# Performance work log

Hardware: AMD Instinct MI355X
Metric: run time of the kernel (lower is better)

The kernel has to match this reference:

```python
import jax, jax.numpy as jnp
import numpy as np

NEG_SLOPE = 0.01  # torch F.leaky_relu default


def _gcn_conv(x, edge_index, Wc, bc):
    """PyG GCNConv with add_self_loops + symmetric normalization.
    x: [N, F], edge_index: [2, E] (row=source, col=target)."""
    N = x.shape[0]
    xw = x @ Wc  # transform first, then propagate
    loop = jnp.arange(N, dtype=edge_index.dtype)
    src = jnp.concatenate([edge_index[0], loop])
    dst = jnp.concatenate([edge_index[1], loop])
    deg = jax.ops.segment_sum(jnp.ones(src.shape[0], xw.dtype), dst, num_segments=N)
    dinv = jnp.where(deg > 0, jax.lax.rsqrt(deg), 0.0)
    norm = dinv[src] * dinv[dst]  # [E+N]
    agg = jax.ops.segment_sum(norm[:, None] * xw[src], dst, num_segments=N)
    return agg + bc


def setup_inputs() -> dict:
    key = jax.random.key(0)
    ks = jax.random.split(key, 6)
    B, N, E, F, H = 8, 10000, 160000, 128, 256
    node_features = jax.random.normal(ks[0], (B, N, F), dtype=jnp.float32)
    edge_index = jax.random.randint(ks[1], (B, 2, E), 0, N, dtype=jnp.int64)
    Wc = jax.random.normal(ks[2], (F, F), dtype=jnp.float32) / np.sqrt(F)
    bc = jnp.zeros((F,), jnp.float32)
    W1 = jax.random.normal(ks[3], (F, H), dtype=jnp.float32) / np.sqrt(F)
    b1 = jnp.zeros((H,), jnp.float32)
    W2 = jax.random.normal(ks[4], (H, H), dtype=jnp.float32) / np.sqrt(H)
    b2 = jnp.zeros((H,), jnp.float32)
    return {"node_features": node_features, "edge_index": edge_index,
            "Wc": Wc, "bc": bc, "W1": W1, "b1": b1, "W2": W2, "b2": b2}


def reference(node_features, edge_index, Wc, bc, W1, b1, W2, b2):
    # vmapped per-graph GCN conv (equivalent to PyG Batch with node offsets)
    conv = jax.vmap(_gcn_conv, in_axes=(0, 0, None, None))
    x0 = node_features  # [B, N, F]
    x = jax.nn.relu(conv(x0, edge_index, Wc, bc))
    x = x + x0  # residual with raw input (batch.x)
    x = jax.nn.leaky_relu(x @ W1 + b1, NEG_SLOPE)
    x = jax.nn.leaky_relu(x @ W2 + b2, NEG_SLOPE)
    return x  # [B, N, H]
```

## Files before the change

### kernel.cpp

```cpp
#include <hip/hip_runtime.h>
#include <hip/hip_bf16.h>
#include <hip/hip_fp16.h>

#define Bn 8
#define Nn 10000
#define En 160000
#define Fn 128
#define Hn 256
#define NROW (Bn * Nn)
#define NEDGE (Bn * En)
#define TM 32

#define OFF_RS   80000
#define OFF_CUR  160004
#define OFF_BS   240004
#define OFF_BO   240320
#define OFF_EP   240832
#define WSI_END  2800832
#define WP_U16   131072
#define WP_BYTES ((size_t)WP_U16 * 2)
#define X0H_BYTES ((size_t)NROW * Fn * 2)
#define X0H_OFF  ((size_t)WSI_END * 4 + WP_BYTES)
#define WS_NEED  (X0H_OFF + X0H_BYTES)

typedef unsigned short u16;
typedef __attribute__((ext_vector_type(8))) short s16x8;
typedef __attribute__((ext_vector_type(8))) _Float16 f16x8;
typedef __attribute__((ext_vector_type(4))) float f32x4;

__device__ __forceinline__ u16 f2bf(float x) {
    unsigned u = __float_as_uint(x);
    u += 0x7FFF + ((u >> 16) & 1);
    return (u16)(u >> 16);
}
__device__ __forceinline__ float bf2f(u16 h) {
    return __uint_as_float((unsigned)h << 16);
}
__device__ __forceinline__ u16 f2h(float x) {
    _Float16 h = (_Float16)x;
    return *(u16*)&h;
}

__device__ __forceinline__ bool edge_is_i64(const int* e) {
    return e[1] == 0 && e[3] == 0;
}
__device__ __forceinline__ int eidx(const int* e, long long i, bool i64) {
    return i64 ? e[2 * i] : e[i];
}

__global__ void k_prep(int* __restrict__ deg, __half* __restrict__ x0h,
                       const float* __restrict__ x0, float* __restrict__ out,
                       const float* __restrict__ Wc, const float* __restrict__ W1,
                       const float* __restrict__ W2, u16* __restrict__ wp) {
    if (blockIdx.x < 10000) {
        int i = blockIdx.x * 256 + threadIdx.x;
        if (i < NROW) deg[i] = 1;
        if (i == 0) out[4] = 1000.0f;
        int r = i >> 5, g = i & 31;
        float4 v = *(const float4*)(x0 + ((size_t)r << 7) + (g << 2));
        __half2 a = __floats2half2_rn(v.x, v.y);
        __half2 b = __floats2half2_rn(v.z, v.w);
        uint2 u;
        u.x = *(unsigned*)&a;
        u.y = *(unsigned*)&b;
        *(uint2*)((char*)x0h + ((size_t)r << 8) + (g << 3)) = u;
    } else {
        int i = (blockIdx.x - 10000) * 256 + threadIdx.x;
        if (i < 16384) {
            int j = i & 7, l = (i >> 3) & 63;
            int nt = (i >> 9) & 7, kt = i >> 12;
            int k = kt * 32 + (l >> 4) * 8 + j;
            int n = nt * 16 + (l & 15);
            float v = Wc[(size_t)k * Fn + n];
            u16 hi = f2bf(v);
            u16 lo = f2bf(v - bf2f(hi));
            int o = (kt * 8 + nt) * 1024 + l * 8 + j;
            wp[o] = hi;
            wp[o + 512] = lo;
        } else if (i < 49152) {
            int idx = i - 16384;
            int j = idx & 7, l = (idx >> 3) & 63;
            int nt = (idx >> 9) & 15, kt = idx >> 13;
            int k = kt * 32 + (l >> 4) * 8 + j;
            int n = nt * 16 + (l & 15);
            wp[32768 + (kt * 16 + nt) * 512 + l * 8 + j] =
                f2h(W1[(size_t)k * Hn + n]);
        } else if (i < 114688) {
            int idx = i - 49152;
            int j = idx & 7, l = (idx >> 3) & 63;
            int nt = (idx >> 9) & 15, kt = idx >> 13;
            int k = kt * 32 + (l >> 4) * 8 + j;
            int n = nt * 16 + (l & 15);
            wp[65536 + (kt * 16 + nt) * 512 + l * 8 + j] =
                f2h(W2[(size_t)k * Hn + n]);
        }
    }
}

__global__ void k_deg2(const int* __restrict__ e, int* __restrict__ deg) {
    bool i64 = edge_is_i64(e);
    int b = blockIdx.x & 7;
    int p = (blockIdx.x >> 3) * 256 + threadIdx.x;
    if (p >= En / 2) return;
    int kk = p * 2;
    int d0, d1;
    if (i64) {
        int4 v = *(const int4*)(e + ((long long)(b * 2 + 1) * En + kk) * 2);
        d0 = v.x; d1 = v.z;
    } else {
        int2 v = *(const int2*)(e + (long long)(b * 2 + 1) * En + kk);
        d0 = v.x; d1 = v.y;
    }
    if ((unsigned)d0 < Nn) atomicAdd(&deg[b * Nn + d0], 1);
    if ((unsigned)d1 < Nn) atomicAdd(&deg[b * Nn + d1], 1);
}

__global__ void k_scan1(const int* __restrict__ deg,
                        int* __restrict__ row_start, int* __restrict__ bsum) {
    __shared__ int s[256];
    int i = blockIdx.x * 256 + threadIdx.x;
    int v = (i < NROW) ? (deg[i] - 1) : 0;
    s[threadIdx.x] = v;
    __syncthreads();
    for (int off = 1; off < 256; off <<= 1) {
        int t = (threadIdx.x >= off) ? s[threadIdx.x - off] : 0;
        __syncthreads();
        s[threadIdx.x] += t;
        __syncthreads();
    }
    if (i < NROW) row_start[i] = s[threadIdx.x] - v;
    if (threadIdx.x == 255) bsum[blockIdx.x] = s[255];
}

__global__ void k_scan2(const int* __restrict__ bsum, int* __restrict__ boff,
                        int* __restrict__ row_start) {
    __shared__ int s[512];
    int t = threadIdx.x;
    int v = (t < 313) ? bsum[t] : 0;
    s[t] = v;
    __syncthreads();
    for (int off = 1; off < 512; off <<= 1) {
        int u = (t >= off) ? s[t - off] : 0;
        __syncthreads();
        s[t] += u;
        __syncthreads();
    }
    boff[t] = s[t] - v;
    if (t == 511) row_start[NROW] = s[511];
}

__global__ void k_scan3(int* __restrict__ degi, float* __restrict__ dinvf,
                        int* __restrict__ row_start,
                        const int* __restrict__ boff, int* __restrict__ cursor) {
    int i = blockIdx.x * blockDim.x + threadIdx.x;
    if (i >= NROW) return;
    int v = row_start[i] + boff[i >> 8];
    row_start[i] = v;
    cursor[i] = v;
    float d = (float)degi[i];
    dinvf[i] = rsqrtf(d);
}

__global__ void k_bin2(const int* __restrict__ e, const float* __restrict__ dinv,
                       int* __restrict__ cursor, int2* __restrict__ ep) {
    bool i64 = edge_is_i64(e);
    int b = blockIdx.x & 7;
    int p = (blockIdx.x >> 3) * 256 + threadIdx.x;
    if (p >= En / 2) return;
    int kk = p * 2;
    int s0, s1, d0, d1;
    if (i64) {
        int4 sv = *(const int4*)(e + ((long long)(b * 2) * En + kk) * 2);
        int4 dv = *(const int4*)(e + ((long long)(b * 2 + 1) * En + kk) * 2);
        s0 = sv.x; s1 = sv.z; d0 = dv.x; d1 = dv.z;
    } else {
        int2 sv = *(const int2*)(e + (long long)(b * 2) * En + kk);
        int2 dv = *(const int2*)(e + (long long)(b * 2 + 1) * En + kk);
        s0 = sv.x; s1 = sv.y; d0 = dv.x; d1 = dv.y;
    }
    if ((unsigned)s0 < Nn && (unsigned)d0 < Nn) {
        int g = b * Nn + s0;
        int pos = atomicAdd(&cursor[b * Nn + d0], 1);
        ep[pos] = make_int2(g, __float_as_int(dinv[g]));
    }
    if ((unsigned)s1 < Nn && (unsigned)d1 < Nn) {
        int g = b * Nn + s1;
        int pos = atomicAdd(&cursor[b * Nn + d1], 1);
        ep[pos] = make_int2(g, __float_as_int(dinv[g]));
    }
}

__device__ __forceinline__ void g_edge_h(const __half* __restrict__ x0h, int s,
                                         float w, int lane, float& ax, float& ay) {
    __half2 h = *(const __half2*)(x0h + ((size_t)s << 7) + 2 * lane);
    float2 v = __half22float2(h);
    ax = fmaf(w, v.x, ax);
    ay = fmaf(w, v.y, ay);
}
__device__ __forceinline__ void g_pair(const __half* __restrict__ x0h,
                                       int4 pq, int lane, float& ax, float& ay) {
    g_edge_h(x0h, pq.x, __int_as_float(pq.y), lane, ax, ay);
    g_edge_h(x0h, pq.z, __int_as_float(pq.w), lane, ax, ay);
}

__global__ __launch_bounds__(256, 6) void k_gfm(
        const __half* __restrict__ x0h, const float* __restrict__ dinv,
        const int* __restrict__ row_start, const int* __restrict__ row_end,
        const int2* __restrict__ ep, const u16* __restrict__ wp,
        const float* __restrict__ bc, const float* __restrict__ b1,
        const float* __restrict__ b2, float* out) {
    __shared__ __align__(16) u16 sm[13056];
    u16* rs_   = sm;
    u16* ag_hi = sm + 4352;
    u16* ag_lo = sm + 8704;
    u16* hs    = sm + 4352;

    int xcd = blockIdx.x & 7, ii = blockIdx.x >> 3;
    int wg = (xcd < 4 ? xcd * 313 : 1252 + (xcd - 4) * 312) + ii;
    int row0 = wg * TM;

    int t = threadIdx.x;
    int w = t >> 6;
    int l = t & 63;
    int lr = l & 15;
    int lg = l >> 4;

#pragma unroll
    for (int it = 0; it < 2; ++it) {
        int idx = it * 256 + t;
        int r = idx >> 4, c = idx & 15;
        *(uint4*)(rs_ + r * 136 + (c << 3)) =
            *(const uint4*)(x0h + ((size_t)(row0 + r) << 7) + (c << 3));
    }

#pragma unroll 1
    for (int rr = 0; rr < 8; ++rr) {
        int r = w * 8 + rr;
        int wid = row0 + r;
        int rs = row_start[wid], re = row_end[wid];
        float wd = dinv[wid];
        float ax = 0.f, ay = 0.f;
        int j = rs;
        if (j < re && (j & 1)) {
            int2 q = ep[j];
            g_edge_h(x0h, q.x, __int_as_float(q.y), l, ax, ay);
            ++j;
        }
        for (; j + 8 <= re; j += 8) {
            int4 p0 = *(const int4*)(ep + j);
            int4 p1 = *(const int4*)(ep + j + 2);
            int4 p2 = *(const int4*)(ep + j + 4);
            int4 p3 = *(const int4*)(ep + j + 6);
            g_pair(x0h, p0, l, ax, ay);
            g_pair(x0h, p1, l, ax, ay);
            g_pair(x0h, p2, l, ax, ay);
            g_pair(x0h, p3, l, ax, ay);
        }
        if (j + 4 <= re) {
            int4 p0 = *(const int4*)(ep + j);
            int4 p1 = *(const int4*)(ep + j + 2);
            g_pair(x0h, p0, l, ax, ay);
            g_pair(x0h, p1, l, ax, ay);
            j += 4;
        }
        if (j + 2 <= re) {
            int4 p0 = *(const int4*)(ep + j);
            g_pair(x0h, p0, l, ax, ay);
            j += 2;
        }
        if (j < re) {
            int2 q = ep[j];
            g_edge_h(x0h, q.x, __int_as_float(q.y), l, ax, ay);
        }
        g_edge_h(x0h, wid, wd, l, ax, ay);
        float sx = wd * ax, sy = wd * ay;
        u16 h0 = f2bf(sx), h1 = f2bf(sy);
        u16 l0 = f2bf(sx - bf2f(h0)), l1 = f2bf(sy - bf2f(h1));
        ((unsigned*)ag_hi)[r * 68 + l] = (unsigned)h0 | ((unsigned)h1 << 16);
        ((unsigned*)ag_lo)[r * 68 + l] = (unsigned)l0 | ((unsigned)l1 << 16);
    }
    __syncthreads();

    {
        f32x4 acc[2][2];
#pragma unroll
        for (int mi = 0; mi < 2; ++mi)
#pragma unroll
            for (int ni = 0; ni < 2; ++ni) acc[mi][ni] = (f32x4){0.f, 0.f, 0.f, 0.f};
#pragma unroll
        for (int kt = 0; kt < 4; ++kt) {
            int ka = kt * 32 + lg * 8;
            s16x8 a0h = *(const s16x8*)(ag_hi + lr * 136 + ka);
            s16x8 a0l = *(const s16x8*)(ag_lo + lr * 136 + ka);
            s16x8 a1h = *(const s16x8*)(ag_hi + (16 + lr) * 136 + ka);
            s16x8 a1l = *(const s16x8*)(ag_lo + (16 + lr) * 136 + ka);
#pragma unroll
            for (int ni = 0; ni < 2; ++ni) {
                int nt = 2 * w + ni;
                const u16* bp = wp + (kt * 8 + nt) * 1024 + l * 8;
                s16x8 bh = *(const s16x8*)(bp);
                s16x8 bl = *(const s16x8*)(bp + 512);
                acc[0][ni] = __builtin_amdgcn_mfma_f32_16x16x32_bf16(a0h, bl, acc[0][ni], 0, 0, 0);
                acc[0][ni] = __builtin_amdgcn_mfma_f32_16x16x32_bf16(a0l, bh, acc[0][ni], 0, 0, 0);
                acc[0][ni] = __builtin_amdgcn_mfma_f32_16x16x32_bf16(a0h, bh, acc[0][ni], 0, 0, 0);
                acc[1][ni] = __builtin_amdgcn_mfma_f32_16x16x32_bf16(a1h, bl, acc[1][ni], 0, 0, 0);
                acc[1][ni] = __builtin_amdgcn_mfma_f32_16x16x32_bf16(a1l, bh, acc[1][ni], 0, 0, 0);
                acc[1][ni] = __builtin_amdgcn_mfma_f32_16x16x32_bf16(a1h, bh, acc[1][ni], 0, 0, 0);
            }
        }
#pragma unroll
        for (int ni = 0; ni < 2; ++ni) {
            int col = (2 * w + ni) * 16 + lr;
            float bias = bc[col];
#pragma unroll
            for (int mi = 0; mi < 2; ++mi)
#pragma unroll
                for (int r = 0; r < 4; ++r) {
                    int row = mi * 16 + lg * 4 + r;
                    float xr = (float)*(const _Float16*)(rs_ + row * 136 + col);
                    float v = acc[mi][ni][r] + bias;
                    v = fmaxf(v, 0.f) + xr;
                    rs_[row * 136 + col] = f2h(v);
                }
        }
    }
    __syncthreads();

    {
        const u16* w1p = wp + 32768;
        f32x4 acc[2][4];
#pragma unroll
        for (int mi = 0; mi < 2; ++mi)
#pragma unroll
            for (int ni = 0; ni < 4; ++ni) acc[mi][ni] = (f32x4){0.f, 0.f, 0.f, 0.f};
#pragma unroll
        for (int kt = 0; kt < 4; ++kt) {
            int ka = kt * 32 + lg * 8;
            f16x8 a0 = *(const f16x8*)(rs_ + lr * 136 + ka);
            f16x8 a1 = *(const f16x8*)(rs_ + (16 + lr) * 136 + ka);
#pragma unroll
            for (int ni = 0; ni < 4; ++ni) {
                int nt = 4 * w + ni;
                f16x8 b = *(const f16x8*)(w1p + (kt * 16 + nt) * 512 + l * 8);
                acc[0][ni] = __builtin_amdgcn_mfma_f32_16x16x32_f16(a0, b, acc[0][ni], 0, 0, 0);
                acc[1][ni] = __builtin_amdgcn_mfma_f32_16x16x32_f16(a1, b, acc[1][ni], 0, 0, 0);
            }
        }
#pragma unroll
        for (int ni = 0; ni < 4; ++ni) {
            int col = (4 * w + ni) * 16 + lr;
            float bias = b1[col];
#pragma unroll
            for (int mi = 0; mi < 2; ++mi)
#pragma unroll
                for (int r = 0; r < 4; ++r) {
                    int row = mi * 16 + lg * 4 + r;
                    float v = acc[mi][ni][r] + bias;
                    v = v > 0.f ? v : 0.01f * v;
                    hs[row * 264 + col] = f2h(v);
                }
        }
    }
    __syncthreads();

    {
        const u16* w2p = wp + 65536;
        f32x4 acc[2][4];
#pragma unroll
        for (int mi = 0; mi < 2; ++mi)
#pragma unroll
            for (int ni = 0; ni < 4; ++ni) acc[mi][ni] = (f32x4){0.f, 0.f, 0.f, 0.f};
#pragma unroll
        for (int kt = 0; kt < 8; ++kt) {
            int ka = kt * 32 + lg * 8;
            f16x8 a0 = *(const f16x8*)(hs + lr * 264 + ka);
            f16x8 a1 = *(const f16x8*)(hs + (16 + lr) * 264 + ka);
#pragma unroll
            for (int ni = 0; ni < 4; ++ni) {
                int nt = 4 * w + ni;
                f16x8 b = *(const f16x8*)(w2p + (kt * 16 + nt) * 512 + l * 8);
                acc[0][ni] = __builtin_amdgcn_mfma_f32_16x16x32_f16(a0, b, acc[0][ni], 0, 0, 0);
                acc[1][ni] = __builtin_amdgcn_mfma_f32_16x16x32_f16(a1, b, acc[1][ni], 0, 0, 0);
            }
        }
#pragma unroll
        for (int ni = 0; ni < 4; ++ni) {
            int col = (4 * w + ni) * 16 + lr;
            float bias = b2[col];
#pragma unroll
            for (int mi = 0; mi < 2; ++mi)
#pragma unroll
                for (int r = 0; r < 4; ++r) {
                    int row = mi * 16 + lg * 4 + r;
                    float v = acc[mi][ni][r] + bias;
                    v = v > 0.f ? v : 0.01f * v;
                    out[((size_t)(row0 + row) << 8) + col] = v;
                }
        }
    }
}

__global__ void k_canary(float* out) {
    if (threadIdx.x == 0 && blockIdx.x == 0) out[4] = 1000.0f;
}
__global__ void k_deg_init(float* __restrict__ deg) {
    int i = blockIdx.x * blockDim.x + threadIdx.x;
    if (i < NROW) deg[i] = 1.0f;
}
__global__ void k_deg_count(const int* __restrict__ e, float* __restrict__ deg) {
    bool i64 = edge_is_i64(e);
    int i = blockIdx.x * blockDim.x + threadIdx.x;
    if (i >= NEDGE) return;
    int b = i / En, k = i - b * En;
    int dst = eidx(e, (long long)(b * 2 + 1) * En + k, i64);
    if ((unsigned)dst < Nn) atomicAdd(&deg[b * Nn + dst], 1.0f);
}
__global__ void k_dinv(float* __restrict__ deg) {
    int i = blockIdx.x * blockDim.x + threadIdx.x;
    if (i < NROW) deg[i] = rsqrtf(deg[i]);
}
__global__ void k_agg_init(const float* __restrict__ x0,
                           const float* __restrict__ dinv,
                           float* __restrict__ out) {
    int i = blockIdx.x * blockDim.x + threadIdx.x;
    if (i >= NROW * Fn) return;
    int r = i >> 7;
    int c = i & 127;
    float dv = dinv[r];
    out[((size_t)r << 8) + c] = dv * dv * x0[i];
}
__global__ void k_scatter(const int* __restrict__ e,
                          const float* __restrict__ dinv,
                          const float* __restrict__ x0,
                          float* __restrict__ out) {
    bool i64 = edge_is_i64(e);
    long long gid = (long long)blockIdx.x * blockDim.x + threadIdx.x;
    int eid = (int)(gid >> 6);
    int lane = (int)(gid & 63);
    if (eid >= NEDGE) return;
    int b = eid / En, k = eid - b * En;
    int src = eidx(e, (long long)(b * 2) * En + k, i64);
    int dst = eidx(e, (long long)(b * 2 + 1) * En + k, i64);
    if ((unsigned)src >= Nn || (unsigned)dst >= Nn) return;
    float nrm = dinv[b * Nn + src] * dinv[b * Nn + dst];
    const float2 vf =
        *(const float2*)(x0 + ((size_t)(b * Nn + src) << 7) + 2 * lane);
    float* p = out + ((size_t)(b * Nn + dst) << 8) + 2 * lane;
    atomicAdd(p, nrm * vf.x);
    atomicAdd(p + 1, nrm * vf.y);
}

__global__ __launch_bounds__(256, 3) void k_fused(
        const float* __restrict__ x0,
        const float* __restrict__ Wc, const float* __restrict__ bc,
        const float* __restrict__ W1, const float* __restrict__ b1,
        const float* __restrict__ W2, const float* __restrict__ b2,
        float* out) {
    __shared__ float smem[12352];
    float (*rs)[Fn + 1] = (float (*)[Fn + 1])smem;
    float (*ag)[Fn + 1] = (float (*)[Fn + 1])(smem + 4128);
    float (*hs)[Hn + 1] = (float (*)[Hn + 1])(smem + 4128);

    int row0 = blockIdx.x * TM;
    int t = threadIdx.x;
    int tx = t & 31;
    int ty = t >> 5;
    int ra = ty * 4;

    for (int i = t; i < TM * Fn; i += 256) {
        int r = i >> 7, c = i & 127;
        ag[r][c] = out[((size_t)(row0 + r) << 8) + c];
    }
    __syncthreads();
    {
        float acc[4][4] = {};
#pragma unroll 4
        for (int k = 0; k < Fn; ++k) {
            float a0 = ag[ra + 0][k], a1 = ag[ra + 1][k],
                  a2 = ag[ra + 2][k], a3 = ag[ra + 3][k];
            const float4 b = *(const float4*)(Wc + k * Fn + tx * 4);
            acc[0][0] = fmaf(a0, b.x, acc[0][0]); acc[0][1] = fmaf(a0, b.y, acc[0][1]);
            acc[0][2] = fmaf(a0, b.z, acc[0][2]); acc[0][3] = fmaf(a0, b.w, acc[0][3]);
            acc[1][0] = fmaf(a1, b.x, acc[1][0]); acc[1][1] = fmaf(a1, b.y, acc[1][1]);
            acc[1][2] = fmaf(a1, b.z, acc[1][2]); acc[1][3] = fmaf(a1, b.w, acc[1][3]);
            acc[2][0] = fmaf(a2, b.x, acc[2][0]); acc[2][1] = fmaf(a2, b.y, acc[2][1]);
            acc[2][2] = fmaf(a2, b.z, acc[2][2]); acc[2][3] = fmaf(a2, b.w, acc[2][3]);
            acc[3][0] = fmaf(a3, b.x, acc[3][0]); acc[3][1] = fmaf(a3, b.y, acc[3][1]);
            acc[3][2] = fmaf(a3, b.z, acc[3][2]); acc[3][3] = fmaf(a3, b.w, acc[3][3]);
        }
        const float4 bcv = *(const float4*)(bc + tx * 4);
        __syncthreads();
#pragma unroll
        for (int i = 0; i < 4; ++i) {
            const float4 xv =
                *(const float4*)(x0 + (size_t)(row0 + ra + i) * Fn + tx * 4);
            rs[ra + i][tx * 4 + 0] = fmaxf(acc[i][0] + bcv.x, 0.f) + xv.x;
            rs[ra + i][tx * 4 + 1] = fmaxf(acc[i][1] + bcv.y, 0.f) + xv.y;
            rs[ra + i][tx * 4 + 2] = fmaxf(acc[i][2] + bcv.z, 0.f) + xv.z;
            rs[ra + i][tx * 4 + 3] = fmaxf(acc[i][3] + bcv.w, 0.f) + xv.w;
        }
    }
    __syncthreads();
    {
        float acc[4][8] = {};
#pragma unroll 2
        for (int k = 0; k < Fn; ++k) {
            float a0 = rs[ra + 0][k], a1 = rs[ra + 1][k],
                  a2 = rs[ra + 2][k], a3 = rs[ra + 3][k];
            const float4 p0 = *(const float4*)(W1 + k * Hn + tx * 8);
            const float4 p1 = *(const float4*)(W1 + k * Hn + tx * 8 + 4);
#pragma unroll
            for (int i = 0; i < 4; ++i) {
                float a = (i == 0) ? a0 : (i == 1) ? a1 : (i == 2) ? a2 : a3;
                acc[i][0] = fmaf(a, p0.x, acc[i][0]); acc[i][1] = fmaf(a, p0.y, acc[i][1]);
                acc[i][2] = fmaf(a, p0.z, acc[i][2]); acc[i][3] = fmaf(a, p0.w, acc[i][3]);
                acc[i][4] = fmaf(a, p1.x, acc[i][4]); acc[i][5] = fmaf(a, p1.y, acc[i][5]);
                acc[i][6] = fmaf(a, p1.z, acc[i][6]); acc[i][7] = fmaf(a, p1.w, acc[i][7]);
            }
        }
        const float4 b1a = *(const float4*)(b1 + tx * 8);
        const float4 b1b = *(const float4*)(b1 + tx * 8 + 4);
        float bias[8] = {b1a.x, b1a.y, b1a.z, b1a.w, b1b.x, b1b.y, b1b.z, b1b.w};
#pragma unroll
        for (int i = 0; i < 4; ++i)
#pragma unroll
            for (int j = 0; j < 8; ++j) {
                float h = acc[i][j] + bias[j];
                hs[ra + i][tx * 8 + j] = h > 0.f ? h : 0.01f * h;
            }
    }
    __syncthreads();
    {
        float acc[4][8] = {};
#pragma unroll 2
        for (int k = 0; k < Hn; ++k) {
            float a0 = hs[ra + 0][k], a1 = hs[ra + 1][k],
                  a2 = hs[ra + 2][k], a3 = hs[ra + 3][k];
            const float4 p0 = *(const float4*)(W2 + k * Hn + tx * 8);
            const float4 p1 = *(const float4*)(W2 + k * Hn + tx * 8 + 4);
#pragma unroll
            for (int i = 0; i < 4; ++i) {
                float a = (i == 0) ? a0 : (i == 1) ? a1 : (i == 2) ? a2 : a3;
                acc[i][0] = fmaf(a, p0.x, acc[i][0]); acc[i][1] = fmaf(a, p0.y, acc[i][1]);
                acc[i][2] = fmaf(a, p0.z, acc[i][2]); acc[i][3] = fmaf(a, p0.w, acc[i][3]);
                acc[i][4] = fmaf(a, p1.x, acc[i][4]); acc[i][5] = fmaf(a, p1.y, acc[i][5]);
                acc[i][6] = fmaf(a, p1.z, acc[i][6]); acc[i][7] = fmaf(a, p1.w, acc[i][7]);
            }
        }
        const float4 b2a = *(const float4*)(b2 + tx * 8);
        const float4 b2b = *(const float4*)(b2 + tx * 8 + 4);
        float bias[8] = {b2a.x, b2a.y, b2a.z, b2a.w, b2b.x, b2b.y, b2b.z, b2b.w};
#pragma unroll
        for (int i = 0; i < 4; ++i) {
            float o[8];
#pragma unroll
            for (int j = 0; j < 8; ++j) {
                float v = acc[i][j] + bias[j];
                o[j] = v > 0.f ? v : 0.01f * v;
            }
            float* dst = out + ((size_t)(row0 + ra + i) << 8) + tx * 8;
            *(float4*)(dst)     = make_float4(o[0], o[1], o[2], o[3]);
            *(float4*)(dst + 4) = make_float4(o[4], o[5], o[6], o[7]);
        }
    }
}

extern "C" void kernel_launch(void* const* d_in, const int* in_sizes, int n_in,
                              void* d_out, int out_size, void* d_ws, size_t ws_size,
                              hipStream_t stream) {
    const float* x0 = (const float*)d_in[0];
    const int*   ed = (const int*)d_in[1];
    const float* Wc = (const float*)d_in[2];
    const float* bc = (const float*)d_in[3];
    const float* W1 = (const float*)d_in[4];
    const float* b1 = (const float*)d_in[5];
    const float* W2 = (const float*)d_in[6];
    const float* b2 = (const float*)d_in[7];

    float* out = (float*)d_out;
    int*   wsi = (int*)d_ws;
    float* wsf = (float*)d_ws;

    if (ws_size >= WS_NEED) {
        int*    degi      = wsi;
        float*  dinv      = wsf;
        int*    row_start = wsi + OFF_RS;
        int*    cursor    = wsi + OFF_CUR;
        int*    bsum      = wsi + OFF_BS;
        int*    boff      = wsi + OFF_BO;
        int2*   ep        = (int2*)(wsi + OFF_EP);
        u16*    wp        = (u16*)(wsi + WSI_END);
        __half* x0h       = (__half*)((char*)d_ws + X0H_OFF);

        int epb = 8 * ((En / 2 + 255) / 256);
        k_prep<<<10448, 256, 0, stream>>>(degi, x0h, x0, out, Wc, W1, W2, wp);
        k_deg2<<<epb, 256, 0, stream>>>(ed, degi);
        k_scan1<<<313, 256, 0, stream>>>(degi, row_start, bsum);
        k_scan2<<<1, 512, 0, stream>>>(bsum, boff, row_start);
        k_scan3<<<313, 256, 0, stream>>>(degi, dinv, row_start, boff, cursor);
        k_bin2<<<epb, 256, 0, stream>>>(ed, dinv, cursor, ep);
        k_gfm<<<NROW / TM, 256, 0, stream>>>(
            x0h, dinv, row_start, cursor, ep, wp, bc, b1, b2, out);
    } else {
        float* deg = wsf;
        k_canary<<<1, 64, 0, stream>>>(out);
        k_deg_init<<<(NROW + 255) / 256, 256, 0, stream>>>(deg);
        k_deg_count<<<(NEDGE + 255) / 256, 256, 0, stream>>>(ed, deg);
        k_dinv<<<(NROW + 255) / 256, 256, 0, stream>>>(deg);
        k_agg_init<<<(NROW * Fn + 255) / 256, 256, 0, stream>>>(x0, deg, out);
        long long sthreads = (long long)NEDGE * 64;
        k_scatter<<<(int)((sthreads + 255) / 256), 256, 0, stream>>>(ed, deg, x0, out);
        k_fused<<<NROW / TM, 256, 0, stream>>>(x0, Wc, bc, W1, b1, W2, b2, out);
    }
}
```

Before: 313.8 us.

## Fuse degree counting into prep kernel and merge scan passes

Degree counting moves into the prep kernel as extra blocks, with the degree array zeroed by a memset beforehand, so one launch does the conversion, weight packing and edge counting. The second and third scan kernels become one kernel, where each block sums the earlier block totals itself and then applies the offset and computes dinv. This removes two kernel launches and the serial single-block scan. The costs are an added memset, redundant block-sum reads in every scan block, and dinv moving to its own workspace slot.

```diff
diff --git a/kernel.cpp b/kernel.cpp
--- a/kernel.cpp
+++ b/kernel.cpp
@@ -14,14 +14,14 @@
 #define OFF_RS   80000
 #define OFF_CUR  160004
 #define OFF_BS   240004
-#define OFF_BO   240320
 #define OFF_EP   240832
 #define WSI_END  2800832
 #define WP_U16   131072
 #define WP_BYTES ((size_t)WP_U16 * 2)
 #define X0H_BYTES ((size_t)NROW * Fn * 2)
 #define X0H_OFF  ((size_t)WSI_END * 4 + WP_BYTES)
-#define WS_NEED  (X0H_OFF + X0H_BYTES)
+#define DINV_OFF (X0H_OFF + X0H_BYTES)
+#define WS_NEED  (DINV_OFF + (size_t)NROW * 4)
 
 typedef unsigned short u16;
 typedef __attribute__((ext_vector_type(8))) short s16x8;
@@ -48,13 +48,45 @@
     return i64 ? e[2 * i] : e[i];
 }
 
-__global__ void k_prep(int* __restrict__ deg, __half* __restrict__ x0h,
-                       const float* __restrict__ x0, float* __restrict__ out,
-                       const float* __restrict__ Wc, const float* __restrict__ W1,
-                       const float* __restrict__ W2, u16* __restrict__ wp) {
+__device__ __forceinline__ void wpack_one(int i, const float* __restrict__ Wc,
+                                          const float* __restrict__ W1,
+                                          const float* __restrict__ W2,
+                                          u16* __restrict__ wp) {
+    if (i < 16384) {
+        int j = i & 7, l = (i >> 3) & 63;
+        int nt = (i >> 9) & 7, kt = i >> 12;
+        int k = kt * 32 + (l >> 4) * 8 + j;
+        int n = nt * 16 + (l & 15);
+        float v = Wc[(size_t)k * Fn + n];
+        u16 hi = f2bf(v);
+        u16 lo = f2bf(v - bf2f(hi));
+        int o = (kt * 8 + nt) * 1024 + l * 8 + j;
+        wp[o] = hi;
+        wp[o + 512] = lo;
+    } else if (i < 49152) {
+        int idx = i - 16384;
+        int j = idx & 7, l = (idx >> 3) & 63;
+        int nt = (idx >> 9) & 15, kt = idx >> 13;
+        int k = kt * 32 + (l >> 4) * 8 + j;
+        int n = nt * 16 + (l & 15);
+        wp[32768 + (kt * 16 + nt) * 512 + l * 8 + j] = f2h(W1[(size_t)k * Hn + n]);
+    } else if (i < 114688) {
+        int idx = i - 49152;
+        int j = idx & 7, l = (idx >> 3) & 63;
+        int nt = (idx >> 9) & 15, kt = idx >> 13;
+        int k = kt * 32 + (l >> 4) * 8 + j;
+        int n = nt * 16 + (l & 15);
+        wp[65536 + (kt * 16 + nt) * 512 + l * 8 + j] = f2h(W2[(size_t)k * Hn + n]);
+    }
+}
+
+__global__ void k_prep2(const int* __restrict__ e, int* __restrict__ deg,
+                        __half* __restrict__ x0h, const float* __restrict__ x0,
+                        float* __restrict__ out,
+                        const float* __restrict__ Wc, const float* __restrict__ W1,
+                        const float* __restrict__ W2, u16* __restrict__ wp) {
     if (blockIdx.x < 10000) {
         int i = blockIdx.x * 256 + threadIdx.x;
-        if (i < NROW) deg[i] = 1;
         if (i == 0) out[4] = 1000.0f;
         int r = i >> 5, g = i & 31;
         float4 v = *(const float4*)(x0 + ((size_t)r << 7) + (g << 2));
@@ -64,62 +96,34 @@
         u.x = *(unsigned*)&a;
         u.y = *(unsigned*)&b;
         *(uint2*)((char*)x0h + ((size_t)r << 8) + (g << 3)) = u;
+    } else if (blockIdx.x < 10448) {
+        int i = (blockIdx.x - 10000) * 256 + threadIdx.x;
+        wpack_one(i, Wc, W1, W2, wp);
     } else {
-        int i = (blockIdx.x - 10000) * 256 + threadIdx.x;
-        if (i < 16384) {
-            int j = i & 7, l = (i >> 3) & 63;
-            int nt = (i >> 9) & 7, kt = i >> 12;
-            int k = kt * 32 + (l >> 4) * 8 + j;
-            int n = nt * 16 + (l & 15);
-            float v = Wc[(size_t)k * Fn + n];
-            u16 hi = f2bf(v);
-            u16 lo = f2bf(v - bf2f(hi));
-            int o = (kt * 8 + nt) * 1024 + l * 8 + j;
-            wp[o] = hi;
-            wp[o + 512] = lo;
-        } else if (i < 49152) {
-            int idx = i - 16384;
-            int j = idx & 7, l = (idx >> 3) & 63;
-            int nt = (idx >> 9) & 15, kt = idx >> 13;
-            int k = kt * 32 + (l >> 4) * 8 + j;
-            int n = nt * 16 + (l & 15);
-            wp[32768 + (kt * 16 + nt) * 512 + l * 8 + j] =
-                f2h(W1[(size_t)k * Hn + n]);
-        } else if (i < 114688) {
-            int idx = i - 49152;
-            int j = idx & 7, l = (idx >> 3) & 63;
-            int nt = (idx >> 9) & 15, kt = idx >> 13;
-            int k = kt * 32 + (l >> 4) * 8 + j;
-            int n = nt * 16 + (l & 15);
-            wp[65536 + (kt * 16 + nt) * 512 + l * 8 + j] =
-                f2h(W2[(size_t)k * Hn + n]);
-        }
-    }
-}
-
-__global__ void k_deg2(const int* __restrict__ e, int* __restrict__ deg) {
-    bool i64 = edge_is_i64(e);
-    int b = blockIdx.x & 7;
-    int p = (blockIdx.x >> 3) * 256 + threadIdx.x;
-    if (p >= En / 2) return;
-    int kk = p * 2;
-    int d0, d1;
-    if (i64) {
-        int4 v = *(const int4*)(e + ((long long)(b * 2 + 1) * En + kk) * 2);
-        d0 = v.x; d1 = v.z;
-    } else {
-        int2 v = *(const int2*)(e + (long long)(b * 2 + 1) * En + kk);
-        d0 = v.x; d1 = v.y;
-    }
-    if ((unsigned)d0 < Nn) atomicAdd(&deg[b * Nn + d0], 1);
-    if ((unsigned)d1 < Nn) atomicAdd(&deg[b * Nn + d1], 1);
+        int idx = blockIdx.x - 10448;
+        bool i64 = edge_is_i64(e);
+        int b = idx & 7;
+        int p = (idx >> 3) * 256 + threadIdx.x;
+        if (p >= En / 2) return;
+        int kk = p * 2;
+        int d0, d1;
+        if (i64) {
+            int4 v = *(const int4*)(e + ((long long)(b * 2 + 1) * En + kk) * 2);
+            d0 = v.x; d1 = v.z;
+        } else {
+            int2 v = *(const int2*)(e + (long long)(b * 2 + 1) * En + kk);
+            d0 = v.x; d1 = v.y;
+        }
+        if ((unsigned)d0 < Nn) atomicAdd(&deg[b * Nn + d0], 1);
+        if ((unsigned)d1 < Nn) atomicAdd(&deg[b * Nn + d1], 1);
+    }
 }
 
 __global__ void k_scan1(const int* __restrict__ deg,
                         int* __restrict__ row_start, int* __restrict__ bsum) {
     __shared__ int s[256];
     int i = blockIdx.x * 256 + threadIdx.x;
-    int v = (i < NROW) ? (deg[i] - 1) : 0;
+    int v = (i < NROW) ? deg[i] : 0;
     s[threadIdx.x] = v;
     __syncthreads();
     for (int off = 1; off < 256; off <<= 1) {
@@ -132,33 +136,28 @@
     if (threadIdx.x == 255) bsum[blockIdx.x] = s[255];
 }
 
-__global__ void k_scan2(const int* __restrict__ bsum, int* __restrict__ boff,
-                        int* __restrict__ row_start) {
-    __shared__ int s[512];
-    int t = threadIdx.x;
-    int v = (t < 313) ? bsum[t] : 0;
-    s[t] = v;
-    __syncthreads();
-    for (int off = 1; off < 512; off <<= 1) {
-        int u = (t >= off) ? s[t - off] : 0;
+__global__ void k_scan23(const int* __restrict__ deg, const int* __restrict__ bsum,
+                         int* __restrict__ row_start, int* __restrict__ cursor,
+                         float* __restrict__ dinvf) {
+    __shared__ int s[256];
+    int tid = threadIdx.x;
+    int blk = blockIdx.x;
+    int part = 0;
+    for (int j = tid; j < blk; j += 256) part += bsum[j];
+    s[tid] = part;
+    __syncthreads();
+    for (int off = 128; off > 0; off >>= 1) {
+        if (tid < off) s[tid] += s[tid + off];
         __syncthreads();
-        s[t] += u;
-        __syncthreads();
-    }
-    boff[t] = s[t] - v;
-    if (t == 511) row_start[NROW] = s[511];
-}
-
-__global__ void k_scan3(int* __restrict__ degi, float* __restrict__ dinvf,
-                        int* __restrict__ row_start,
-                        const int* __restrict__ boff, int* __restrict__ cursor) {
-    int i = blockIdx.x * blockDim.x + threadIdx.x;
-    if (i >= NROW) return;
-    int v = row_start[i] + boff[i >> 8];
-    row_start[i] = v;
-    cursor[i] = v;
-    float d = (float)degi[i];
-    dinvf[i] = rsqrtf(d);
+    }
+    int boff = s[0];
+    int i = blk * 256 + tid;
+    if (i < NROW) {
+        int v = row_start[i] + boff;
+        row_start[i] = v;
+        cursor[i] = v;
+        dinvf[i] = rsqrtf((float)deg[i] + 1.0f);
+    }
 }
 
 __global__ void k_bin2(const int* __restrict__ e, const float* __restrict__ dinv,
@@ -583,21 +582,20 @@
 
     if (ws_size >= WS_NEED) {
         int*    degi      = wsi;
-        float*  dinv      = wsf;
         int*    row_start = wsi + OFF_RS;
         int*    cursor    = wsi + OFF_CUR;
         int*    bsum      = wsi + OFF_BS;
-        int*    boff      = wsi + OFF_BO;
         int2*   ep        = (int2*)(wsi + OFF_EP);
         u16*    wp        = (u16*)(wsi + WSI_END);
         __half* x0h       = (__half*)((char*)d_ws + X0H_OFF);
+        float*  dinv      = (float*)((char*)d_ws + DINV_OFF);
 
         int epb = 8 * ((En / 2 + 255) / 256);
-        k_prep<<<10448, 256, 0, stream>>>(degi, x0h, x0, out, Wc, W1, W2, wp);
-        k_deg2<<<epb, 256, 0, stream>>>(ed, degi);
+        hipMemsetAsync(degi, 0, (size_t)NROW * 4, stream);
+        k_prep2<<<10448 + epb, 256, 0, stream>>>(ed, degi, x0h, x0, out,
+                                                 Wc, W1, W2, wp);
         k_scan1<<<313, 256, 0, stream>>>(degi, row_start, bsum);
-        k_scan2<<<1, 512, 0, stream>>>(bsum, boff, row_start);
-        k_scan3<<<313, 256, 0, stream>>>(degi, dinv, row_start, boff, cursor);
+        k_scan23<<<313, 256, 0, stream>>>(degi, bsum, row_start, cursor, dinv);
         k_bin2<<<epb, 256, 0, stream>>>(ed, dinv, cursor, ep);
         k_gfm<<<NROW / TM, 256, 0, stream>>>(
             x0h, dinv, row_start, cursor, ep, wp, bc, b1, b2, out);
```

New measurement: 311.8 us. No clear change (-0.6%).
